# Performance work log

Hardware: AMD Instinct MI355X
Metric: run time of the kernel (lower is better)

The kernel has to match this reference:

```python
import jax, jax.numpy as jnp
import numpy as np

B, L, E, H = 2, 2048, 1024, 16
HD = E // H          # head_dim = 64
G = H // 4           # heads per kernel-size group = 4


def _dwconv(x, w, b):
    """Causal depthwise conv. x: (B, G, L, D); w: (D, k); b: (D,).
    Matches PadLeft(k-1) + Conv1d(D, D, k, groups=D): y[l] = sum_j w[:, j] * x[l - (k-1) + j] + b."""
    k = w.shape[-1]
    Lx = x.shape[2]
    xp = jnp.pad(x, ((0, 0), (0, 0), (k - 1, 0), (0, 0)))
    out = b
    for j in range(k):
        out = out + xp[:, :, j:j + Lx, :] * w[:, j]
    return out


def setup_inputs() -> dict:
    key = jax.random.key(0)
    ks = jax.random.split(key, 32)
    s = 0.02
    inp = {"x": jax.random.normal(ks[0], (B, L, E), jnp.float32)}
    for i, n in enumerate(["Wq", "Wk", "Wv", "Wo"]):
        inp[n] = jax.random.normal(ks[1 + i], (E, E), jnp.float32) * s
    inp["bo"] = jax.random.normal(ks[5], (E,), jnp.float32) * s
    i = 6
    for ksz in (3, 5, 7):
        for pfx in ("q", "k", "v"):
            inp[f"{pfx}{ksz}_w"] = jax.random.normal(ks[i], (HD, ksz), jnp.float32) * (1.0 / ksz)
            inp[f"{pfx}{ksz}_b"] = jax.random.normal(ks[i + 1], (HD,), jnp.float32) * s
            i += 2
    return inp


def reference(x, Wq, Wk, Wv, Wo, bo,
              q3_w, q3_b, k3_w, k3_b, v3_w, v3_b,
              q5_w, q5_b, k5_w, k5_b, v5_w, v5_b,
              q7_w, q7_b, k7_w, k7_b, v7_w, v7_b):
    b, l, _ = x.shape

    def split(t):  # (b, l, E) -> (b, 4, G, l, HD)
        return t.reshape(b, l, 4, G, HD).transpose(0, 2, 3, 1, 4)

    q = split(x @ Wq.T)
    k = split(x @ Wk.T)
    v = split(x @ Wv.T)

    # NOTE: faithful to source quirks -- k and v convs are applied to the
    # (already convolved) q group, not to k/v.
    q0, k0, v0 = q[:, 0], k[:, 0], v[:, 0]
    q1 = _dwconv(q[:, 1], q3_w, q3_b)
    k1 = _dwconv(q1, k3_w, k3_b)
    v1 = _dwconv(q1, v3_w, v3_b)
    q2 = _dwconv(q[:, 2], q5_w, q5_b)
    k2 = _dwconv(q2, k5_w, k5_b)
    v2 = _dwconv(q2, v5_w, v5_b)
    q3 = _dwconv(q[:, 3], q7_w, q7_b)
    k3 = _dwconv(q3, k7_w, k7_b)
    v3 = _dwconv(q3, v7_w, v7_b)

    Q = jnp.concatenate([q0, q1, q2, q3], axis=1)  # (b, H, l, HD)
    K = jnp.concatenate([k0, k1, k2, k3], axis=1)
    V = jnp.concatenate([v0, v1, v2, v3], axis=1)

    logit = jnp.einsum('bnid,bnjd->bnij', Q, K) * (HD ** -0.5)
    attn = jax.nn.softmax(logit, axis=-1)
    attn_out = jnp.einsum('bnij,bnjd->bnid', attn, V)

    # Source quirk: output uses rearranged V, discarding attn_out.
    out = V.transpose(0, 2, 1, 3).reshape(b, l, E)
    # keep the attention compute alive without changing the math
    out = out + 0.0 * attn_out.transpose(0, 2, 1, 3).reshape(b, l, E)
    return out @ Wo.T + bo
```

## Files before the change

kernel.cpp:

```cpp
#include <hip/hip_runtime.h>
#include <hip/hip_bf16.h>
#include <stdint.h>

#define L_SEQ 2048
#define MTOT  4096
#define EDIM  1024

typedef __attribute__((ext_vector_type(8))) short bf16x8;
typedef __attribute__((ext_vector_type(4))) float f32x4;
typedef __attribute__((ext_vector_type(4))) float float4v;
typedef __attribute__((ext_vector_type(4))) unsigned short us4;
typedef __attribute__((ext_vector_type(2))) unsigned int u32x2;

__device__ __forceinline__ unsigned short f2b(float f) {
    union { float f; unsigned u; } v; v.f = f;
    return (unsigned short)((v.u + 0x7FFFu + ((v.u >> 16) & 1u)) >> 16);
}
__device__ __forceinline__ float b2f(unsigned short h) {
    union { unsigned u; float f; } v; v.u = ((unsigned)h) << 16;
    return v.f;
}

__device__ __forceinline__ void lds16(const void* g, void* l) {
    __builtin_amdgcn_global_load_lds((const __attribute__((address_space(1))) void*)g,
                                     (__attribute__((address_space(3))) void*)l, 16, 0, 0);
}

__global__ __launch_bounds__(256) void prep_kernel(
    const float* __restrict__ x, const float* __restrict__ Wq,
    const float* __restrict__ Wv, const float* __restrict__ Wo,
    unsigned short* __restrict__ xb, unsigned short* __restrict__ W1b,
    unsigned short* __restrict__ Wob,
    const float* __restrict__ q3w, const float* __restrict__ q3b,
    const float* __restrict__ v3w, const float* __restrict__ v3b,
    const float* __restrict__ q5w, const float* __restrict__ q5b,
    const float* __restrict__ v5w, const float* __restrict__ v5b,
    const float* __restrict__ q7w, const float* __restrict__ q7b,
    const float* __restrict__ v7w, const float* __restrict__ v7b,
    float* __restrict__ H, float* __restrict__ Beff, float* __restrict__ Corr)
{
    const int XQ = (MTOT * EDIM) / 4;
    const int WQ = (EDIM * EDIM) / 4;
    if (blockIdx.x >= 6144) {
        int ch = (blockIdx.x - 6144) * 256 + threadIdx.x;
        int g = ch >> 8;
        int d = ch & 63;
        int k = 3 + 2 * g;
        const float* qw = (g == 0) ? q3w : (g == 1) ? q5w : q7w;
        const float* qb = (g == 0) ? q3b : (g == 1) ? q5b : q7b;
        const float* vw = (g == 0) ? v3w : (g == 1) ? v5w : v7w;
        const float* vb = (g == 0) ? v3b : (g == 1) ? v5b : v7b;

        float hq[7], hv[7];
        for (int i = 0; i < 7; ++i) { hq[i] = 0.f; hv[i] = 0.f; }
        for (int i = 0; i < k; ++i) {
            hq[i] = qw[d * k + (k - 1 - i)];
            hv[i] = vw[d * k + (k - 1 - i)];
        }
        float h[13];
        for (int i = 0; i < 13; ++i) h[i] = 0.f;
        for (int a = 0; a < 7; ++a)
            for (int b = 0; b < 7; ++b)
                h[a + b] += hq[a] * hv[b];
        for (int i = 0; i < 13; ++i) H[i * 768 + ch] = h[i];

        float sv = 0.f;
        for (int j = 0; j < k; ++j) sv += vw[d * k + j];
        Beff[ch] = qb[d] * sv + vb[d];

        for (int l = 0; l < 6; ++l) {
            float s2 = 0.f;
            for (int i = l + 1; i < 7; ++i) s2 += hv[i];
            Corr[l * 768 + ch] = qb[d] * s2;
        }
        return;
    }
    int i = blockIdx.x * 256 + threadIdx.x;
    const float* src;
    unsigned short* dst;
    int j;
    if (i < XQ) {
        j = i * 4; src = x; dst = xb;
    } else if (i < XQ + WQ) {
        j = (i - XQ) * 4;
        int row = j >> 10;
        src = (row < 256) ? Wv : Wq;
        dst = W1b;
    } else {
        j = (i - XQ - WQ) * 4; src = Wo; dst = Wob;
    }
    float4v v = *(const float4v*)(src + j);
    us4 o;
    o[0] = f2b(v[0]); o[1] = f2b(v[1]); o[2] = f2b(v[2]); o[3] = f2b(v[3]);
    *(us4*)(dst + j) = o;
}

template <int OUT_MODE>
__global__ __launch_bounds__(512, 2) void gemm_ks(
    const unsigned short* __restrict__ A, const unsigned short* __restrict__ BT,
    unsigned short* __restrict__ Cb, float* __restrict__ Cf,
    const float* __restrict__ bias, int M, int N, int K)
{
    __shared__ unsigned short sh[3 * 16384];

    const int nbx = N >> 7;
    int orig = blockIdx.y * nbx + blockIdx.x;
    int nwg  = (M >> 7) * nbx;
    int wg   = (orig & 7) * (nwg >> 3) + (orig >> 3);
    const int m0 = (wg / nbx) * 128, n0 = (wg % nbx) * 128;

    const int tid  = threadIdx.x;
    const int wid  = tid >> 6;
    const int lane = tid & 63;
    const int wr   = wid >> 2;
    const int wc   = (wid >> 1) & 1;
    const int kh   = wid & 1;
    const int fr   = lane & 15, fq = lane >> 4;

    f32x4 acc[4][4] = {};

    const unsigned short* Aptr = A  + (size_t)m0 * K;
    const unsigned short* Bptr = BT + (size_t)n0 * K;

    const size_t offA0 = (size_t)(tid >> 3) * K + (((tid & 7) ^ ((tid >> 3) & 7)) * 8);
    const size_t offA1 = offA0 + (size_t)64 * K;

    auto stage = [&](int buf, int t) {
        unsigned short* Al = sh + buf * 16384;
        unsigned short* Bl = Al + 8192;
        const unsigned short* Ag = Aptr + (t << 6);
        const unsigned short* Bg = Bptr + (t << 6);
        lds16(Ag + offA0, Al + tid * 8);
        lds16(Ag + offA1, Al + (512 + tid) * 8);
        lds16(Bg + offA0, Bl + tid * 8);
        lds16(Bg + offA1, Bl + (512 + tid) * 8);
    };

    auto compute = [&](int buf) {
        const unsigned short* as = sh + buf * 16384;
        const unsigned short* bs = as + 8192;
        bf16x8 a[4], b[4];
#pragma unroll
        for (int mi = 0; mi < 4; ++mi) {
            int row = wr * 64 + mi * 16 + fr;
            a[mi] = *(const bf16x8*)(as + row * 64 + (((kh * 4 + fq) ^ (row & 7)) * 8));
        }
#pragma unroll
        for (int ni = 0; ni < 4; ++ni) {
            int row = wc * 64 + ni * 16 + fr;
            b[ni] = *(const bf16x8*)(bs + row * 64 + (((kh * 4 + fq) ^ (row & 7)) * 8));
        }
#pragma unroll
        for (int mi = 0; mi < 4; ++mi)
#pragma unroll
            for (int ni = 0; ni < 4; ++ni)
                acc[mi][ni] = __builtin_amdgcn_mfma_f32_16x16x32_bf16(a[mi], b[ni], acc[mi][ni], 0, 0, 0);
    };

    const int NT = K >> 6;
    stage(0, 0);
    stage(1, 1);
    asm volatile("s_waitcnt vmcnt(4)" ::: "memory");
    __builtin_amdgcn_s_barrier();
    asm volatile("" ::: "memory");

    for (int t = 0; t < NT; ++t) {
        if (t + 2 < NT) stage((t + 2) % 3, t + 2);
        compute(t % 3);
        if (t + 1 < NT) {
            if (t + 2 < NT) {
                asm volatile("s_waitcnt vmcnt(4)" ::: "memory");
            } else {
                asm volatile("s_waitcnt vmcnt(0)" ::: "memory");
            }
            __builtin_amdgcn_s_barrier();
            asm volatile("" ::: "memory");
        }
    }

    __syncthreads();
    float* Mg = (float*)sh;
    const int mgbase = (wr * 2 + wc) * 4096;
    if (kh) {
#pragma unroll
        for (int mi = 0; mi < 4; ++mi)
#pragma unroll
            for (int ni = 0; ni < 4; ++ni) {
                int col = ni * 16 + fr;
                int adr = mgbase + col * 64 + (((mi * 4 + fq) ^ (col & 15)) << 2);
                *(f32x4*)(Mg + adr) = acc[mi][ni];
            }
    }
    __syncthreads();
    if (!kh) {
#pragma unroll
        for (int mi = 0; mi < 4; ++mi) {
#pragma unroll
            for (int ni = 0; ni < 4; ++ni) {
                int col = ni * 16 + fr;
                int adr = mgbase + col * 64 + (((mi * 4 + fq) ^ (col & 15)) << 2);
                f32x4 p = *(const f32x4*)(Mg + adr);
                int gcol = n0 + wc * 64 + col;
                int rowb = m0 + wr * 64 + mi * 16 + fq * 4;
#pragma unroll
                for (int j = 0; j < 4; ++j) {
                    float v = acc[mi][ni][j] + p[j];
                    if (OUT_MODE == 0) {
                        Cb[(size_t)(rowb + j) * N + gcol] = f2b(v);
                    } else {
                        Cf[(size_t)(rowb + j) * N + gcol] = v + bias[gcol];
                    }
                }
            }
        }
    }
}

__global__ __launch_bounds__(256) void conv_kernel(
    const unsigned short* __restrict__ T, unsigned short* __restrict__ V,
    const float* __restrict__ H, const float* __restrict__ Beff,
    const float* __restrict__ Corr)
{
    int w  = blockIdx.x * 256 + threadIdx.x;
    int m  = (w >> 8) * 2;
    int e0 = (w & 255) * 4;
    const unsigned short* tp = T + (size_t)m * EDIM + e0;
    unsigned short*       vp = V + (size_t)m * EDIM + e0;
    if (e0 < 256) {
        *(u32x2*)vp = *(const u32x2*)tp;
        *(u32x2*)(vp + EDIM) = *(const u32x2*)(tp + EDIM);
        return;
    }
    int l  = m & (L_SEQ - 1);
    int ch = e0 - 256;
    float4v b4 = *(const float4v*)(Beff + ch);
    float4v acc0 = b4, acc1 = b4;

    {
        float4v h = *(const float4v*)(H + ch);
        us4 t = *(const us4*)(tp + EDIM);
        acc1[0] += h[0] * b2f(t[0]); acc1[1] += h[1] * b2f(t[1]);
        acc1[2] += h[2] * b2f(t[2]); acc1[3] += h[3] * b2f(t[3]);
    }
    int ni = (l < 12) ? l : 12;
    for (int i = 0; i <= ni; ++i) {
        us4 t = *(const us4*)(tp - (size_t)i * EDIM);
        float4v h0 = *(const float4v*)(H + i * 768 + ch);
        acc0[0] += h0[0] * b2f(t[0]); acc0[1] += h0[1] * b2f(t[1]);
        acc0[2] += h0[2] * b2f(t[2]); acc0[3] += h0[3] * b2f(t[3]);
        if (i < 12) {
            float4v h1 = *(const float4v*)(H + (i + 1) * 768 + ch);
            acc1[0] += h1[0] * b2f(t[0]); acc1[1] += h1[1] * b2f(t[1]);
            acc1[2] += h1[2] * b2f(t[2]); acc1[3] += h1[3] * b2f(t[3]);
        }
    }
    if (l < 6) {
        float4v c = *(const float4v*)(Corr + l * 768 + ch);
        acc0[0] -= c[0]; acc0[1] -= c[1]; acc0[2] -= c[2]; acc0[3] -= c[3];
    }
    if (l + 1 < 6) {
        float4v c = *(const float4v*)(Corr + (l + 1) * 768 + ch);
        acc1[0] -= c[0]; acc1[1] -= c[1]; acc1[2] -= c[2]; acc1[3] -= c[3];
    }
    us4 o0, o1;
    o0[0] = f2b(acc0[0]); o0[1] = f2b(acc0[1]); o0[2] = f2b(acc0[2]); o0[3] = f2b(acc0[3]);
    o1[0] = f2b(acc1[0]); o1[1] = f2b(acc1[1]); o1[2] = f2b(acc1[2]); o1[3] = f2b(acc1[3]);
    *(us4*)vp = o0;
    *(us4*)(vp + EDIM) = o1;
}

extern "C" void kernel_launch(void* const* d_in, const int* in_sizes, int n_in,
                              void* d_out, int out_size, void* d_ws, size_t ws_size,
                              hipStream_t stream)
{
    const float* x  = (const float*)d_in[0];
    const float* Wq = (const float*)d_in[1];
    const float* Wv = (const float*)d_in[3];
    const float* Wo = (const float*)d_in[4];
    const float* bo = (const float*)d_in[5];

    uint8_t* ws = (uint8_t*)d_ws;
    unsigned short* xb  = (unsigned short*)(ws);
    unsigned short* W1b = (unsigned short*)(ws + (8u  << 20));
    unsigned short* Wob = (unsigned short*)(ws + (10u << 20));
    unsigned short* T   = (unsigned short*)(ws + (12u << 20));
    unsigned short* V   = (unsigned short*)(ws + (20u << 20));
    float* H    = (float*)(ws + (28u << 20));
    float* Beff = (float*)(ws + (28u << 20) + (64u << 10));
    float* Corr = (float*)(ws + (28u << 20) + (96u << 10));

    prep_kernel<<<6147, 256, 0, stream>>>(
        x, Wq, Wv, Wo, xb, W1b, Wob,
        (const float*)d_in[6],  (const float*)d_in[7],
        (const float*)d_in[10], (const float*)d_in[11],
        (const float*)d_in[12], (const float*)d_in[13],
        (const float*)d_in[16], (const float*)d_in[17],
        (const float*)d_in[18], (const float*)d_in[19],
        (const float*)d_in[22], (const float*)d_in[23],
        H, Beff, Corr);

    dim3 gg(EDIM / 128, MTOT / 128);
    gemm_ks<0><<<gg, 512, 0, stream>>>(xb, W1b, T, nullptr, nullptr, MTOT, EDIM, EDIM);

    conv_kernel<<<2048, 256, 0, stream>>>(T, V, H, Beff, Corr);

    gemm_ks<1><<<gg, 512, 0, stream>>>(V, Wob, nullptr, (float*)d_out, bo, MTOT, EDIM, EDIM);
}
```

Baseline: 55.61 us.

## Fuse x fp32-to-bf16 conversion into GEMM A-load with register-staged pipeline

Drops the separate pass that converts x to bf16. The first GEMM now reads fp32 x directly, packs it to bf16 in registers and writes it to LDS. The GEMMs switch from direct global-to-LDS loads with triple buffering to register-staged double buffering with a two-deep register prefetch. The tile shrinks to 128x64 and launch bounds rise to 4 waves/SIMD, doubling the workgroup count. This saves one full read/write of x, at the cost of more barriers, more VGPR pressure and twice the fp32 A-read bandwidth in the first GEMM.

```diff
diff --git a/kernel.cpp b/kernel.cpp
--- a/kernel.cpp
+++ b/kernel.cpp
@@ -20,17 +20,19 @@
     union { unsigned u; float f; } v; v.u = ((unsigned)h) << 16;
     return v.f;
 }
-
-__device__ __forceinline__ void lds16(const void* g, void* l) {
-    __builtin_amdgcn_global_load_lds((const __attribute__((address_space(1))) void*)g,
-                                     (__attribute__((address_space(3))) void*)l, 16, 0, 0);
-}
-
-__global__ __launch_bounds__(256) void prep_kernel(
-    const float* __restrict__ x, const float* __restrict__ Wq,
-    const float* __restrict__ Wv, const float* __restrict__ Wo,
-    unsigned short* __restrict__ xb, unsigned short* __restrict__ W1b,
-    unsigned short* __restrict__ Wob,
+__device__ __forceinline__ bf16x8 pack8(f32x4 lo, f32x4 hi) {
+    bf16x8 o;
+    o[0] = (short)f2b(lo[0]); o[1] = (short)f2b(lo[1]);
+    o[2] = (short)f2b(lo[2]); o[3] = (short)f2b(lo[3]);
+    o[4] = (short)f2b(hi[0]); o[5] = (short)f2b(hi[1]);
+    o[6] = (short)f2b(hi[2]); o[7] = (short)f2b(hi[3]);
+    return o;
+}
+
+__global__ __launch_bounds__(256) void wprep_kernel(
+    const float* __restrict__ Wq, const float* __restrict__ Wv,
+    const float* __restrict__ Wo,
+    unsigned short* __restrict__ W1b, unsigned short* __restrict__ Wob,
     const float* __restrict__ q3w, const float* __restrict__ q3b,
     const float* __restrict__ v3w, const float* __restrict__ v3b,
     const float* __restrict__ q5w, const float* __restrict__ q5b,
@@ -39,10 +41,8 @@
     const float* __restrict__ v7w, const float* __restrict__ v7b,
     float* __restrict__ H, float* __restrict__ Beff, float* __restrict__ Corr)
 {
-    const int XQ = (MTOT * EDIM) / 4;
-    const int WQ = (EDIM * EDIM) / 4;
-    if (blockIdx.x >= 6144) {
-        int ch = (blockIdx.x - 6144) * 256 + threadIdx.x;
+    if (blockIdx.x >= 2048) {
+        int ch = (blockIdx.x - 2048) * 256 + threadIdx.x;
         int g = ch >> 8;
         int d = ch & 63;
         int k = 3 + 2 * g;
@@ -75,19 +75,18 @@
         }
         return;
     }
+    const int WQ = (EDIM * EDIM) / 4;
     int i = blockIdx.x * 256 + threadIdx.x;
     const float* src;
     unsigned short* dst;
     int j;
-    if (i < XQ) {
-        j = i * 4; src = x; dst = xb;
-    } else if (i < XQ + WQ) {
-        j = (i - XQ) * 4;
+    if (i < WQ) {
+        j = i * 4;
         int row = j >> 10;
         src = (row < 256) ? Wv : Wq;
         dst = W1b;
     } else {
-        j = (i - XQ - WQ) * 4; src = Wo; dst = Wob;
+        j = (i - WQ) * 4; src = Wo; dst = Wob;
     }
     float4v v = *(const float4v*)(src + j);
     us4 o;
@@ -95,19 +94,20 @@
     *(us4*)(dst + j) = o;
 }
 
-template <int OUT_MODE>
-__global__ __launch_bounds__(512, 2) void gemm_ks(
-    const unsigned short* __restrict__ A, const unsigned short* __restrict__ BT,
+template <int TA, int OUT_MODE>
+__global__ __launch_bounds__(512, 4) void gemm_rs(
+    const float* __restrict__ Af, const unsigned short* __restrict__ Ab,
+    const unsigned short* __restrict__ BT,
     unsigned short* __restrict__ Cb, float* __restrict__ Cf,
     const float* __restrict__ bias, int M, int N, int K)
 {
-    __shared__ unsigned short sh[3 * 16384];
-
-    const int nbx = N >> 7;
+    __shared__ unsigned short sh[2 * 12288];
+
+    const int nbx = N >> 6;
     int orig = blockIdx.y * nbx + blockIdx.x;
     int nwg  = (M >> 7) * nbx;
     int wg   = (orig & 7) * (nwg >> 3) + (orig >> 3);
-    const int m0 = (wg / nbx) * 128, n0 = (wg % nbx) * 128;
+    const int m0 = (wg / nbx) * 128, n0 = (wg % nbx) * 64;
 
     const int tid  = threadIdx.x;
     const int wid  = tid >> 6;
@@ -117,77 +117,104 @@
     const int kh   = wid & 1;
     const int fr   = lane & 15, fq = lane >> 4;
 
-    f32x4 acc[4][4] = {};
-
-    const unsigned short* Aptr = A  + (size_t)m0 * K;
-    const unsigned short* Bptr = BT + (size_t)n0 * K;
-
-    const size_t offA0 = (size_t)(tid >> 3) * K + (((tid & 7) ^ ((tid >> 3) & 7)) * 8);
-    const size_t offA1 = offA0 + (size_t)64 * K;
-
-    auto stage = [&](int buf, int t) {
-        unsigned short* Al = sh + buf * 16384;
-        unsigned short* Bl = Al + 8192;
-        const unsigned short* Ag = Aptr + (t << 6);
-        const unsigned short* Bg = Bptr + (t << 6);
-        lds16(Ag + offA0, Al + tid * 8);
-        lds16(Ag + offA1, Al + (512 + tid) * 8);
-        lds16(Bg + offA0, Bl + tid * 8);
-        lds16(Bg + offA1, Bl + (512 + tid) * 8);
-    };
+    f32x4 acc[4][2] = {};
+
+    const int r = tid >> 3, g = tid & 7;
+    const int dstA0 = r * 64 + ((g ^ (r & 7)) * 8);
+    const int dstA1 = dstA0 + 64 * 64;
+    const int dstB  = dstA0;
+
+    const size_t gA = (size_t)(m0 + r) * K + g * 8;
+    const size_t gA2 = gA + (size_t)64 * K;
+    const size_t gB = (size_t)(n0 + r) * K + g * 8;
+
+    f32x4 al0_0, ah0_0, al1_0, ah1_0; bf16x8 aa0_0, aa1_0, bb_0;
+    f32x4 al0_1, ah0_1, al1_1, ah1_1; bf16x8 aa0_1, aa1_1, bb_1;
+
+#define LOADBANK(BK_, t_) do {                                            \
+        if (TA == 1) {                                                    \
+            const float* Ag = Af + gA + ((t_) << 6);                      \
+            al0_##BK_ = *(const f32x4*)(Ag);                              \
+            ah0_##BK_ = *(const f32x4*)(Ag + 4);                          \
+            al1_##BK_ = *(const f32x4*)(Af + gA2 + ((t_) << 6));          \
+            ah1_##BK_ = *(const f32x4*)(Af + gA2 + ((t_) << 6) + 4);      \
+        } else {                                                          \
+            aa0_##BK_ = *(const bf16x8*)(Ab + gA + ((t_) << 6));          \
+            aa1_##BK_ = *(const bf16x8*)(Ab + gA2 + ((t_) << 6));         \
+        }                                                                 \
+        bb_##BK_ = *(const bf16x8*)(BT + gB + ((t_) << 6));               \
+    } while (0)
+
+#define DSWRITE(BK_, buf_) do {                                           \
+        unsigned short* Al = sh + (buf_) * 12288;                         \
+        unsigned short* Bl = Al + 8192;                                   \
+        if (TA == 1) {                                                    \
+            *(bf16x8*)(Al + dstA0) = pack8(al0_##BK_, ah0_##BK_);         \
+            *(bf16x8*)(Al + dstA1) = pack8(al1_##BK_, ah1_##BK_);         \
+        } else {                                                          \
+            *(bf16x8*)(Al + dstA0) = aa0_##BK_;                           \
+            *(bf16x8*)(Al + dstA1) = aa1_##BK_;                           \
+        }                                                                 \
+        *(bf16x8*)(Bl + dstB) = bb_##BK_;                                 \
+        asm volatile("s_waitcnt lgkmcnt(0)" ::: "memory");                \
+    } while (0)
 
     auto compute = [&](int buf) {
-        const unsigned short* as = sh + buf * 16384;
+        const unsigned short* as = sh + buf * 12288;
         const unsigned short* bs = as + 8192;
-        bf16x8 a[4], b[4];
+        bf16x8 a[4], b[2];
 #pragma unroll
         for (int mi = 0; mi < 4; ++mi) {
             int row = wr * 64 + mi * 16 + fr;
             a[mi] = *(const bf16x8*)(as + row * 64 + (((kh * 4 + fq) ^ (row & 7)) * 8));
         }
 #pragma unroll
-        for (int ni = 0; ni < 4; ++ni) {
-            int row = wc * 64 + ni * 16 + fr;
+        for (int ni = 0; ni < 2; ++ni) {
+            int row = wc * 32 + ni * 16 + fr;
             b[ni] = *(const bf16x8*)(bs + row * 64 + (((kh * 4 + fq) ^ (row & 7)) * 8));
         }
 #pragma unroll
         for (int mi = 0; mi < 4; ++mi)
 #pragma unroll
-            for (int ni = 0; ni < 4; ++ni)
+            for (int ni = 0; ni < 2; ++ni)
                 acc[mi][ni] = __builtin_amdgcn_mfma_f32_16x16x32_bf16(a[mi], b[ni], acc[mi][ni], 0, 0, 0);
     };
 
     const int NT = K >> 6;
-    stage(0, 0);
-    stage(1, 1);
-    asm volatile("s_waitcnt vmcnt(4)" ::: "memory");
+    LOADBANK(0, 0);
+    LOADBANK(1, 1);
+    DSWRITE(0, 0);
+    LOADBANK(0, 2);
+    DSWRITE(1, 1);
+    LOADBANK(1, 3);
     __builtin_amdgcn_s_barrier();
-    asm volatile("" ::: "memory");
-
-    for (int t = 0; t < NT; ++t) {
-        if (t + 2 < NT) stage((t + 2) % 3, t + 2);
-        compute(t % 3);
-        if (t + 1 < NT) {
-            if (t + 2 < NT) {
-                asm volatile("s_waitcnt vmcnt(4)" ::: "memory");
-            } else {
-                asm volatile("s_waitcnt vmcnt(0)" ::: "memory");
-            }
-            __builtin_amdgcn_s_barrier();
-            asm volatile("" ::: "memory");
-        }
-    }
+
+    for (int tt = 0; tt < NT; tt += 2) {
+        compute(0);
+        __builtin_amdgcn_s_barrier();
+        if (tt + 2 < NT) DSWRITE(0, 0);
+        if (tt + 4 < NT) LOADBANK(0, tt + 4);
+        __builtin_amdgcn_s_barrier();
+
+        compute(1);
+        __builtin_amdgcn_s_barrier();
+        if (tt + 3 < NT) DSWRITE(1, 1);
+        if (tt + 5 < NT) LOADBANK(1, tt + 5);
+        __builtin_amdgcn_s_barrier();
+    }
+#undef LOADBANK
+#undef DSWRITE
 
     __syncthreads();
     float* Mg = (float*)sh;
-    const int mgbase = (wr * 2 + wc) * 4096;
+    const int mgq = (wr * 2 + wc) * 2048;
     if (kh) {
 #pragma unroll
         for (int mi = 0; mi < 4; ++mi)
 #pragma unroll
-            for (int ni = 0; ni < 4; ++ni) {
+            for (int ni = 0; ni < 2; ++ni) {
                 int col = ni * 16 + fr;
-                int adr = mgbase + col * 64 + (((mi * 4 + fq) ^ (col & 15)) << 2);
+                int adr = mgq + col * 64 + (((mi * 4 + fq) ^ (col & 15)) << 2);
                 *(f32x4*)(Mg + adr) = acc[mi][ni];
             }
     }
@@ -196,11 +223,11 @@
 #pragma unroll
         for (int mi = 0; mi < 4; ++mi) {
 #pragma unroll
-            for (int ni = 0; ni < 4; ++ni) {
+            for (int ni = 0; ni < 2; ++ni) {
                 int col = ni * 16 + fr;
-                int adr = mgbase + col * 64 + (((mi * 4 + fq) ^ (col & 15)) << 2);
+                int adr = mgq + col * 64 + (((mi * 4 + fq) ^ (col & 15)) << 2);
                 f32x4 p = *(const f32x4*)(Mg + adr);
-                int gcol = n0 + wc * 64 + col;
+                int gcol = n0 + wc * 32 + col;
                 int rowb = m0 + wr * 64 + mi * 16 + fq * 4;
 #pragma unroll
                 for (int j = 0; j < 4; ++j) {
@@ -280,17 +307,16 @@
     const float* bo = (const float*)d_in[5];
 
     uint8_t* ws = (uint8_t*)d_ws;
-    unsigned short* xb  = (unsigned short*)(ws);
-    unsigned short* W1b = (unsigned short*)(ws + (8u  << 20));
-    unsigned short* Wob = (unsigned short*)(ws + (10u << 20));
-    unsigned short* T   = (unsigned short*)(ws + (12u << 20));
-    unsigned short* V   = (unsigned short*)(ws + (20u << 20));
-    float* H    = (float*)(ws + (28u << 20));
-    float* Beff = (float*)(ws + (28u << 20) + (64u << 10));
-    float* Corr = (float*)(ws + (28u << 20) + (96u << 10));
-
-    prep_kernel<<<6147, 256, 0, stream>>>(
-        x, Wq, Wv, Wo, xb, W1b, Wob,
+    unsigned short* W1b = (unsigned short*)(ws);
+    unsigned short* Wob = (unsigned short*)(ws + (2u  << 20));
+    unsigned short* T   = (unsigned short*)(ws + (4u  << 20));
+    unsigned short* V   = (unsigned short*)(ws + (12u << 20));
+    float* H    = (float*)(ws + (20u << 20));
+    float* Beff = (float*)(ws + (20u << 20) + (64u << 10));
+    float* Corr = (float*)(ws + (20u << 20) + (96u << 10));
+
+    wprep_kernel<<<2051, 256, 0, stream>>>(
+        Wq, Wv, Wo, W1b, Wob,
         (const float*)d_in[6],  (const float*)d_in[7],
         (const float*)d_in[10], (const float*)d_in[11],
         (const float*)d_in[12], (const float*)d_in[13],
@@ -299,10 +325,12 @@
         (const float*)d_in[22], (const float*)d_in[23],
         H, Beff, Corr);
 
-    dim3 gg(EDIM / 128, MTOT / 128);
-    gemm_ks<0><<<gg, 512, 0, stream>>>(xb, W1b, T, nullptr, nullptr, MTOT, EDIM, EDIM);
+    dim3 gg(EDIM / 64, MTOT / 128);
+    gemm_rs<1, 0><<<gg, 512, 0, stream>>>(x, nullptr, W1b, T, nullptr, nullptr,
+                                          MTOT, EDIM, EDIM);
 
     conv_kernel<<<2048, 256, 0, stream>>>(T, V, H, Beff, Corr);
 
-    gemm_ks<1><<<gg, 512, 0, stream>>>(V, Wob, nullptr, (float*)d_out, bo, MTOT, EDIM, EDIM);
-}
+    gemm_rs<0, 1><<<gg, 512, 0, stream>>>(nullptr, V, Wob, nullptr, (float*)d_out, bo,
+                                          MTOT, EDIM, EDIM);
+}
```

New measurement: 59.46 us. +6.9%, slower.

## Fuse fp32-to-bf16 conversion of x into first GEMM and skip passthrough copy

Applied to the files above, without the earlier changes.

The first GEMM now loads fp32 x tiles straight into LDS and converts them to bf16 in registers with packed cvt instructions, so the separate x conversion pass and its bf16 buffer go away. The conv kernel no longer copies the unconvolved first head group into V. Instead, the second GEMM reads A from T for the first k-tiles and from V for the rest. This cuts memory traffic and launch work, but the first GEMM uses double the LDS for its A tiles, which may reduce occupancy.

```diff
diff --git a/kernel.cpp b/kernel.cpp
--- a/kernel.cpp
+++ b/kernel.cpp
@@ -10,7 +10,6 @@
 typedef __attribute__((ext_vector_type(4))) float f32x4;
 typedef __attribute__((ext_vector_type(4))) float float4v;
 typedef __attribute__((ext_vector_type(4))) unsigned short us4;
-typedef __attribute__((ext_vector_type(2))) unsigned int u32x2;
 
 __device__ __forceinline__ unsigned short f2b(float f) {
     union { float f; unsigned u; } v; v.f = f;
@@ -20,17 +19,21 @@
     union { unsigned u; float f; } v; v.u = ((unsigned)h) << 16;
     return v.f;
 }
+__device__ __forceinline__ unsigned cvtpk(float lo, float hi) {
+    unsigned r;
+    asm("v_cvt_pk_bf16_f32 %0, %1, %2" : "=v"(r) : "v"(lo), "v"(hi));
+    return r;
+}
 
 __device__ __forceinline__ void lds16(const void* g, void* l) {
     __builtin_amdgcn_global_load_lds((const __attribute__((address_space(1))) void*)g,
                                      (__attribute__((address_space(3))) void*)l, 16, 0, 0);
 }
 
-__global__ __launch_bounds__(256) void prep_kernel(
-    const float* __restrict__ x, const float* __restrict__ Wq,
-    const float* __restrict__ Wv, const float* __restrict__ Wo,
-    unsigned short* __restrict__ xb, unsigned short* __restrict__ W1b,
-    unsigned short* __restrict__ Wob,
+__global__ __launch_bounds__(256) void wprep_kernel(
+    const float* __restrict__ Wq, const float* __restrict__ Wv,
+    const float* __restrict__ Wo,
+    unsigned short* __restrict__ W1b, unsigned short* __restrict__ Wob,
     const float* __restrict__ q3w, const float* __restrict__ q3b,
     const float* __restrict__ v3w, const float* __restrict__ v3b,
     const float* __restrict__ q5w, const float* __restrict__ q5b,
@@ -39,10 +42,8 @@
     const float* __restrict__ v7w, const float* __restrict__ v7b,
     float* __restrict__ H, float* __restrict__ Beff, float* __restrict__ Corr)
 {
-    const int XQ = (MTOT * EDIM) / 4;
-    const int WQ = (EDIM * EDIM) / 4;
-    if (blockIdx.x >= 6144) {
-        int ch = (blockIdx.x - 6144) * 256 + threadIdx.x;
+    if (blockIdx.x >= 2048) {
+        int ch = (blockIdx.x - 2048) * 256 + threadIdx.x;
         int g = ch >> 8;
         int d = ch & 63;
         int k = 3 + 2 * g;
@@ -75,19 +76,18 @@
         }
         return;
     }
+    const int WQ = (EDIM * EDIM) / 4;
     int i = blockIdx.x * 256 + threadIdx.x;
     const float* src;
     unsigned short* dst;
     int j;
-    if (i < XQ) {
-        j = i * 4; src = x; dst = xb;
-    } else if (i < XQ + WQ) {
-        j = (i - XQ) * 4;
+    if (i < WQ) {
+        j = i * 4;
         int row = j >> 10;
         src = (row < 256) ? Wv : Wq;
         dst = W1b;
     } else {
-        j = (i - XQ - WQ) * 4; src = Wo; dst = Wob;
+        j = (i - WQ) * 4; src = Wo; dst = Wob;
     }
     float4v v = *(const float4v*)(src + j);
     us4 o;
@@ -95,19 +95,22 @@
     *(us4*)(dst + j) = o;
 }
 
-template <int OUT_MODE>
-__global__ __launch_bounds__(512, 2) void gemm_ks(
-    const unsigned short* __restrict__ A, const unsigned short* __restrict__ BT,
+template <int TA, int OUT_MODE>
+__global__ __launch_bounds__(512, 2) void gemm_f(
+    const float* __restrict__ Af,
+    const unsigned short* __restrict__ Ab0, const unsigned short* __restrict__ Ab1,
+    int tsplit,
+    const unsigned short* __restrict__ BT,
     unsigned short* __restrict__ Cb, float* __restrict__ Cf,
-    const float* __restrict__ bias, int M, int N, int K)
+    const float* __restrict__ bias)
 {
-    __shared__ unsigned short sh[3 * 16384];
-
-    const int nbx = N >> 7;
-    int orig = blockIdx.y * nbx + blockIdx.x;
-    int nwg  = (M >> 7) * nbx;
-    int wg   = (orig & 7) * (nwg >> 3) + (orig >> 3);
-    const int m0 = (wg / nbx) * 128, n0 = (wg % nbx) * 128;
+    constexpr int ABUF = TA ? 49152 : 32768;
+    constexpr int ABYT = TA ? 32768 : 16384;
+    __shared__ uint8_t sh[3 * ABUF];
+
+    int orig = blockIdx.y * 8 + blockIdx.x;
+    int wg   = (orig & 7) * 32 + (orig >> 3);
+    const int m0 = (wg >> 3) * 128, n0 = (wg & 7) * 128;
 
     const int tid  = threadIdx.x;
     const int wid  = tid >> 6;
@@ -119,31 +122,59 @@
 
     f32x4 acc[4][4] = {};
 
-    const unsigned short* Aptr = A  + (size_t)m0 * K;
-    const unsigned short* Bptr = BT + (size_t)n0 * K;
-
-    const size_t offA0 = (size_t)(tid >> 3) * K + (((tid & 7) ^ ((tid >> 3) & 7)) * 8);
-    const size_t offA1 = offA0 + (size_t)64 * K;
-
     auto stage = [&](int buf, int t) {
-        unsigned short* Al = sh + buf * 16384;
-        unsigned short* Bl = Al + 8192;
-        const unsigned short* Ag = Aptr + (t << 6);
-        const unsigned short* Bg = Bptr + (t << 6);
-        lds16(Ag + offA0, Al + tid * 8);
-        lds16(Ag + offA1, Al + (512 + tid) * 8);
-        lds16(Bg + offA0, Bl + tid * 8);
-        lds16(Bg + offA1, Bl + (512 + tid) * 8);
+        uint8_t* Abase = sh + buf * ABUF;
+        uint8_t* Bbase = Abase + ABYT;
+        if (TA) {
+            const float* Asrc = Af + (size_t)m0 * EDIM + t * 64;
+#pragma unroll
+            for (int j = 0; j < 4; ++j) {
+                int slot = j * 512 + tid;
+                int row = slot >> 4, c = (slot & 15) ^ (row & 15);
+                lds16(Asrc + (size_t)row * EDIM + c * 4,
+                      Abase + j * 8192 + wid * 1024);
+            }
+        } else {
+            const unsigned short* Asrc =
+                (t < tsplit ? Ab0 : Ab1) + (size_t)m0 * EDIM + t * 64;
+#pragma unroll
+            for (int j = 0; j < 2; ++j) {
+                int slot = j * 512 + tid;
+                int row = slot >> 3, c = (slot & 7) ^ (row & 7);
+                lds16(Asrc + (size_t)row * EDIM + c * 8,
+                      Abase + j * 8192 + wid * 1024);
+            }
+        }
+        const unsigned short* Bsrc = BT + (size_t)n0 * EDIM + t * 64;
+#pragma unroll
+        for (int j = 0; j < 2; ++j) {
+            int slot = j * 512 + tid;
+            int row = slot >> 3, c = (slot & 7) ^ (row & 7);
+            lds16(Bsrc + (size_t)row * EDIM + c * 8,
+                  Bbase + j * 8192 + wid * 1024);
+        }
     };
 
     auto compute = [&](int buf) {
-        const unsigned short* as = sh + buf * 16384;
-        const unsigned short* bs = as + 8192;
+        const uint8_t* Abase = sh + buf * ABUF;
+        const unsigned short* bs = (const unsigned short*)(Abase + ABYT);
         bf16x8 a[4], b[4];
 #pragma unroll
         for (int mi = 0; mi < 4; ++mi) {
             int row = wr * 64 + mi * 16 + fr;
-            a[mi] = *(const bf16x8*)(as + row * 64 + (((kh * 4 + fq) ^ (row & 7)) * 8));
+            if (TA) {
+                const float* as = (const float*)Abase;
+                int c0 = kh * 8 + fq * 2;
+                f32x4 lo = *(const f32x4*)(as + row * 64 + ((c0 ^ (row & 15)) * 4));
+                f32x4 hi = *(const f32x4*)(as + row * 64 + (((c0 + 1) ^ (row & 15)) * 4));
+                union { unsigned u[4]; bf16x8 v; } fu;
+                fu.u[0] = cvtpk(lo[0], lo[1]); fu.u[1] = cvtpk(lo[2], lo[3]);
+                fu.u[2] = cvtpk(hi[0], hi[1]); fu.u[3] = cvtpk(hi[2], hi[3]);
+                a[mi] = fu.v;
+            } else {
+                const unsigned short* as = (const unsigned short*)Abase;
+                a[mi] = *(const bf16x8*)(as + row * 64 + (((kh * 4 + fq) ^ (row & 7)) * 8));
+            }
         }
 #pragma unroll
         for (int ni = 0; ni < 4; ++ni) {
@@ -157,10 +188,11 @@
                 acc[mi][ni] = __builtin_amdgcn_mfma_f32_16x16x32_bf16(a[mi], b[ni], acc[mi][ni], 0, 0, 0);
     };
 
-    const int NT = K >> 6;
+    const int NT = EDIM >> 6;
     stage(0, 0);
     stage(1, 1);
-    asm volatile("s_waitcnt vmcnt(4)" ::: "memory");
+    if (TA) asm volatile("s_waitcnt vmcnt(6)" ::: "memory");
+    else    asm volatile("s_waitcnt vmcnt(4)" ::: "memory");
     __builtin_amdgcn_s_barrier();
     asm volatile("" ::: "memory");
 
@@ -169,7 +201,8 @@
         compute(t % 3);
         if (t + 1 < NT) {
             if (t + 2 < NT) {
-                asm volatile("s_waitcnt vmcnt(4)" ::: "memory");
+                if (TA) asm volatile("s_waitcnt vmcnt(6)" ::: "memory");
+                else    asm volatile("s_waitcnt vmcnt(4)" ::: "memory");
             } else {
                 asm volatile("s_waitcnt vmcnt(0)" ::: "memory");
             }
@@ -206,9 +239,9 @@
                 for (int j = 0; j < 4; ++j) {
                     float v = acc[mi][ni][j] + p[j];
                     if (OUT_MODE == 0) {
-                        Cb[(size_t)(rowb + j) * N + gcol] = f2b(v);
+                        Cb[(size_t)(rowb + j) * EDIM + gcol] = f2b(v);
                     } else {
-                        Cf[(size_t)(rowb + j) * N + gcol] = v + bias[gcol];
+                        Cf[(size_t)(rowb + j) * EDIM + gcol] = v + bias[gcol];
                     }
                 }
             }
@@ -221,18 +254,15 @@
     const float* __restrict__ H, const float* __restrict__ Beff,
     const float* __restrict__ Corr)
 {
-    int w  = blockIdx.x * 256 + threadIdx.x;
-    int m  = (w >> 8) * 2;
-    int e0 = (w & 255) * 4;
+    unsigned w  = blockIdx.x * 256 + threadIdx.x;
+    unsigned rp = w / 192u;
+    int c4 = (int)(w - rp * 192u);
+    int m  = (int)rp * 2;
+    int ch = c4 * 4;
+    int e0 = 256 + ch;
     const unsigned short* tp = T + (size_t)m * EDIM + e0;
     unsigned short*       vp = V + (size_t)m * EDIM + e0;
-    if (e0 < 256) {
-        *(u32x2*)vp = *(const u32x2*)tp;
-        *(u32x2*)(vp + EDIM) = *(const u32x2*)(tp + EDIM);
-        return;
-    }
     int l  = m & (L_SEQ - 1);
-    int ch = e0 - 256;
     float4v b4 = *(const float4v*)(Beff + ch);
     float4v acc0 = b4, acc1 = b4;
 
@@ -280,17 +310,16 @@
     const float* bo = (const float*)d_in[5];
 
     uint8_t* ws = (uint8_t*)d_ws;
-    unsigned short* xb  = (unsigned short*)(ws);
-    unsigned short* W1b = (unsigned short*)(ws + (8u  << 20));
-    unsigned short* Wob = (unsigned short*)(ws + (10u << 20));
-    unsigned short* T   = (unsigned short*)(ws + (12u << 20));
-    unsigned short* V   = (unsigned short*)(ws + (20u << 20));
-    float* H    = (float*)(ws + (28u << 20));
-    float* Beff = (float*)(ws + (28u << 20) + (64u << 10));
-    float* Corr = (float*)(ws + (28u << 20) + (96u << 10));
-
-    prep_kernel<<<6147, 256, 0, stream>>>(
-        x, Wq, Wv, Wo, xb, W1b, Wob,
+    unsigned short* W1b = (unsigned short*)(ws);
+    unsigned short* Wob = (unsigned short*)(ws + (2u  << 20));
+    unsigned short* T   = (unsigned short*)(ws + (4u  << 20));
+    unsigned short* V   = (unsigned short*)(ws + (12u << 20));
+    float* H    = (float*)(ws + (20u << 20));
+    float* Beff = (float*)(ws + (20u << 20) + (64u << 10));
+    float* Corr = (float*)(ws + (20u << 20) + (96u << 10));
+
+    wprep_kernel<<<2051, 256, 0, stream>>>(
+        Wq, Wv, Wo, W1b, Wob,
         (const float*)d_in[6],  (const float*)d_in[7],
         (const float*)d_in[10], (const float*)d_in[11],
         (const float*)d_in[12], (const float*)d_in[13],
@@ -300,9 +329,11 @@
         H, Beff, Corr);
 
     dim3 gg(EDIM / 128, MTOT / 128);
-    gemm_ks<0><<<gg, 512, 0, stream>>>(xb, W1b, T, nullptr, nullptr, MTOT, EDIM, EDIM);
-
-    conv_kernel<<<2048, 256, 0, stream>>>(T, V, H, Beff, Corr);
-
-    gemm_ks<1><<<gg, 512, 0, stream>>>(V, Wob, nullptr, (float*)d_out, bo, MTOT, EDIM, EDIM);
-}
+    gemm_f<1, 0><<<gg, 512, 0, stream>>>(x, nullptr, nullptr, 0,
+                                         W1b, T, nullptr, nullptr);
+
+    conv_kernel<<<1536, 256, 0, stream>>>(T, V, H, Beff, Corr);
+
+    gemm_f<0, 1><<<gg, 512, 0, stream>>>(nullptr, T, V, 4,
+                                         Wob, nullptr, (float*)d_out, bo);
+}
```

New measurement: 53.42 us. -3.9%, faster.
